# Optimization experiments

Hardware: AMD Instinct MI355X
Metric: run time of the kernel (lower is better)

Reference implementation:

```python
import jax, jax.numpy as jnp
import numpy as np

N_NODES = 50000
N_EDGES = 800000
HIDDEN = 64


def _init_linear(key, fan_in, fan_out):
    kw, kb = jax.random.split(key)
    lim = 1.0 / np.sqrt(fan_in)
    W = jax.random.uniform(kw, (fan_in, fan_out), jnp.float32, -lim, lim)
    b = jax.random.uniform(kb, (fan_out,), jnp.float32, -lim, lim)
    return W, b


def setup_inputs() -> dict:
    key = jax.random.key(0)
    ks = jax.random.split(key, 10)
    feat = jax.random.normal(ks[0], (N_NODES, HIDDEN), jnp.float32)
    x = jax.random.normal(ks[1], (N_NODES, 3), jnp.float32)
    src = jax.random.randint(ks[2], (N_EDGES,), 0, N_NODES, jnp.int32)
    dst = jax.random.randint(ks[3], (N_EDGES,), 0, N_NODES, jnp.int32)
    # message MLP: (2H+1) -> H -> H, relu after both layers (last_activation=mid)
    W1, b1 = _init_linear(ks[4], 2 * HIDDEN + 1, HIDDEN)
    W2, b2 = _init_linear(ks[5], HIDDEN, HIDDEN)
    # soft edge gate: H -> 1
    we, be = _init_linear(ks[6], HIDDEN, 1)
    # update MLP: H -> H -> H, relu mid, no last activation
    U1, c1 = _init_linear(ks[7], HIDDEN, HIDDEN)
    U2, c2 = _init_linear(ks[8], HIDDEN, HIDDEN)
    return dict(feat=feat, x=x, src=src, dst=dst,
                W1=W1, b1=b1, W2=W2, b2=b2, we=we, be=be,
                U1=U1, c1=c1, U2=U2, c2=c2)


def reference(feat, x, src, dst, W1, b1, W2, b2, we, be, U1, c1, U2, c2):
    # per-edge squared distance between endpoint coordinates: [E, 1]
    sqd = jnp.sum((x[src] - x[dst]) ** 2, axis=-1, keepdims=True)
    # message input: [E, 2H+1]
    msg_in = jnp.concatenate([feat[src], feat[dst], sqd], axis=-1)
    # 2-layer message MLP with relu mid and last activation
    m = jax.nn.relu(jax.nn.relu(msg_in @ W1 + b1) @ W2 + b2)
    # sigmoid soft-edge gate: [E, 1]
    gate = jax.nn.sigmoid(m @ we + be)
    # scatter-sum gated messages to destination nodes: [N, H]
    m_sum = jax.ops.segment_sum(m * gate, dst, num_segments=N_NODES)
    # node update MLP on (m_sum + feat), residual add
    h = m_sum + feat
    h_new = jax.nn.relu(h @ U1 + c1) @ U2 + c2
    return h_new + feat
```

## Files before the change

### kernel.cpp

```cpp
#include <hip/hip_runtime.h>
#include <hip/hip_bf16.h>
#include <stdint.h>

#define N_NODES 50000
#define N_EDGES 800000
#define HDIM 64
#define SCAN_N (N_NODES + 1)

#define MSUM_OFF   0
#define DEG_OFF    12800000
#define ZERO_BYTES (DEG_OFF + 204800)
#define PART_OFF   (DEG_OFF + 204800)
#define OFFS_OFF   (PART_OFF + 1024)
#define POS_OFF    (OFFS_OFF + 204800)
#define EP_OFF     (POS_OFF + 204800)
#define FB_OFF     (EP_OFF + 12800000)
#define W1T_OFF    (FB_OFF + (size_t)N_NODES * HDIM * 2)
#define W2T_OFF    (W1T_OFF + 16384)
#define U1T_OFF    (W2T_OFF + 8192)
#define U2T_OFF    (U1T_OFF + 8192)
#define CST_OFF    (U2T_OFF + 8192)
#define WS_NEED    (CST_OFF + 4096)

#define CVT_BLOCKS   1563
#define PREPW_BLOCKS 82
#define HIST_BLOCKS  1024

typedef __attribute__((ext_vector_type(8))) short short8;
typedef __attribute__((ext_vector_type(4))) float floatx4;

__device__ __forceinline__ float bf2f(unsigned short u) {
    union { unsigned int i; float f; } v; v.i = ((unsigned int)u) << 16; return v.f;
}
__device__ __forceinline__ unsigned short f2bf(float f) {
    __hip_bfloat16 h = __float2bfloat16(f);
    return *reinterpret_cast<unsigned short*>(&h);
}

__device__ __forceinline__ int detect_is_bf16(const unsigned short* p) {
    int cnt = 0;
    #pragma unroll
    for (int i = 0; i < 64; ++i) {
        unsigned short b = p[i];
        int e = (b >> 7) & 0xFF;
        cnt += ((e >= 97 && e <= 157) || (b & 0x7FFF) == 0) ? 1 : 0;
    }
    return cnt >= 56;
}

__device__ __forceinline__ float getf(const void* p, unsigned int i, int isb) {
    return isb ? bf2f(((const unsigned short*)p)[i]) : ((const float*)p)[i];
}

__device__ __forceinline__ short8 get8bf(const void* p, unsigned int i, int isb) {
    if (isb) {
        return *reinterpret_cast<const short8*>((const short*)p + i);
    } else {
        const float4 f0 = *reinterpret_cast<const float4*>((const float*)p + i);
        const float4 f1 = *reinterpret_cast<const float4*>((const float*)p + i + 4);
        short8 a;
        a[0] = (short)f2bf(f0.x); a[1] = (short)f2bf(f0.y);
        a[2] = (short)f2bf(f0.z); a[3] = (short)f2bf(f0.w);
        a[4] = (short)f2bf(f1.x); a[5] = (short)f2bf(f1.y);
        a[6] = (short)f2bf(f1.z); a[7] = (short)f2bf(f1.w);
        return a;
    }
}

#define COMPILER_FENCE() asm volatile("" ::: "memory")
#define WAIT_LDS() __builtin_amdgcn_s_waitcnt(0xC07F)

__global__ __launch_bounds__(256) void prep_kernel(
    const void* __restrict__ feat, unsigned short* __restrict__ fb,
    const void* __restrict__ W1, const void* __restrict__ W2,
    const void* __restrict__ U1, const void* __restrict__ U2,
    const void* __restrict__ b1, const void* __restrict__ b2,
    const void* __restrict__ we, const void* __restrict__ be,
    unsigned short* __restrict__ w1t, unsigned short* __restrict__ w2t,
    unsigned short* __restrict__ u1t, unsigned short* __restrict__ u2t,
    float* __restrict__ cst,
    const int* __restrict__ dst, int* __restrict__ deg)
{
    const int b = blockIdx.x;
    if (b < CVT_BLOCKS) {
        const int isb = detect_is_bf16((const unsigned short*)feat);
        int i = (b * 256 + threadIdx.x) * 8;
        if (i >= N_NODES * HDIM) return;
        if (isb) {
            *reinterpret_cast<uint4*>(fb + i) =
                *reinterpret_cast<const uint4*>((const unsigned short*)feat + i);
        } else {
            float4 f0 = *reinterpret_cast<const float4*>((const float*)feat + i);
            float4 f1 = *reinterpret_cast<const float4*>((const float*)feat + i + 4);
            ushort4 a = {f2bf(f0.x), f2bf(f0.y), f2bf(f0.z), f2bf(f0.w)};
            ushort4 c = {f2bf(f1.x), f2bf(f1.y), f2bf(f1.z), f2bf(f1.w)};
            *reinterpret_cast<ushort4*>(fb + i)     = a;
            *reinterpret_cast<ushort4*>(fb + i + 4) = c;
        }
    } else if (b < CVT_BLOCKS + PREPW_BLOCKS) {
        const int isb = detect_is_bf16((const unsigned short*)feat);
        int idx = (b - CVT_BLOCKS) * 256 + threadIdx.x;
        if (idx < 8192) {
            int n = idx >> 7, k = idx & 127;
            w1t[idx] = f2bf(getf(W1, k * 64 + n, isb));
        } else if (idx < 12288) {
            int i = idx - 8192, n = i >> 6, k = i & 63;
            w2t[i] = f2bf(getf(W2, k * 64 + n, isb));
        } else if (idx < 16384) {
            int i = idx - 12288, n = i >> 6, k = i & 63;
            u1t[i] = f2bf(getf(U1, k * 64 + n, isb));
        } else if (idx < 20480) {
            int i = idx - 16384, n = i >> 6, k = i & 63;
            u2t[i] = f2bf(getf(U2, k * 64 + n, isb));
        } else if (idx < 20737) {
            int i = idx - 20480;
            float v;
            if (i < 64)       v = getf(b1, i, isb);
            else if (i < 128) v = getf(W1, 128 * 64 + (i - 64), isb);
            else if (i < 192) v = getf(b2, i - 128, isb);
            else if (i < 256) v = getf(we, i - 192, isb);
            else              v = getf(be, 0, isb);
            cst[i] = v;
        }
    } else {
        int e0 = (b - CVT_BLOCKS - PREPW_BLOCKS) * 256 + threadIdx.x;
        for (int e = e0; e < N_EDGES; e += HIST_BLOCKS * 256)
            atomicAdd(&deg[dst[e]], 1);
    }
}

__global__ void scan1_kernel(const int* __restrict__ deg, int* __restrict__ part) {
    __shared__ int s[1024];
    int g = blockIdx.x * 1024 + threadIdx.x;
    s[threadIdx.x] = (g < SCAN_N) ? deg[g] : 0;
    __syncthreads();
    for (int off = 512; off > 0; off >>= 1) {
        if (threadIdx.x < off) s[threadIdx.x] += s[threadIdx.x + off];
        __syncthreads();
    }
    if (threadIdx.x == 0) part[blockIdx.x] = s[0];
}

__global__ void scan3_kernel(const int* __restrict__ deg, const int* __restrict__ part,
                             int* __restrict__ offs, int* __restrict__ pos) {
    __shared__ int s[1024];
    __shared__ int sbase;
    if (threadIdx.x < 64) {
        int v = (threadIdx.x < blockIdx.x) ? part[threadIdx.x] : 0;
        #pragma unroll
        for (int off = 32; off >= 1; off >>= 1) v += __shfl_xor(v, off);
        if (threadIdx.x == 0) sbase = v;
    }
    int g = blockIdx.x * 1024 + threadIdx.x;
    int v = (g < SCAN_N) ? deg[g] : 0;
    s[threadIdx.x] = v;
    __syncthreads();
    for (int off = 1; off < 1024; off <<= 1) {
        int t = (threadIdx.x >= off) ? s[threadIdx.x - off] : 0;
        __syncthreads();
        s[threadIdx.x] += t;
        __syncthreads();
    }
    int excl = s[threadIdx.x] - v + sbase;
    if (g < SCAN_N) { offs[g] = excl; pos[g] = excl; }
}

__global__ __launch_bounds__(256) void permute_kernel(
    const void* __restrict__ feat, const void* __restrict__ xpos,
    const int* __restrict__ src, const int* __restrict__ dst,
    int* __restrict__ pos, uint4* __restrict__ epack)
{
    const int isb = detect_is_bf16((const unsigned short*)feat);
    int e = blockIdx.x * 256 + threadIdx.x;
    if (e < N_EDGES) {
        int s = src[e], d = dst[e];
        int slot = atomicAdd(&pos[d], 1);
        float dx = getf(xpos, s * 3 + 0, isb) - getf(xpos, d * 3 + 0, isb);
        float dy = getf(xpos, s * 3 + 1, isb) - getf(xpos, d * 3 + 1, isb);
        float dz = getf(xpos, s * 3 + 2, isb) - getf(xpos, d * 3 + 2, isb);
        float sqd = dx * dx + dy * dy + dz * dz;
        uint4 p;
        p.x = (unsigned int)s;
        p.y = (unsigned int)d;
        p.z = __float_as_uint(sqd);
        p.w = 0u;
        epack[slot] = p;
    }
}

template <bool CSR>
__global__ __launch_bounds__(512, 4) void edge_kernel(
    const unsigned short* __restrict__ fbf,
    const unsigned short* __restrict__ w1t, const unsigned short* __restrict__ w2t,
    const float* __restrict__ cst,
    const void* __restrict__ feat, const void* __restrict__ xpos,
    const int* __restrict__ src, const int* __restrict__ dst,
    const uint4* __restrict__ epack,
    const void* __restrict__ W1, const void* __restrict__ b1,
    const void* __restrict__ W2, const void* __restrict__ b2,
    const void* __restrict__ we, const void* __restrict__ be,
    float* __restrict__ msum, unsigned int msum_cap)
{
    __shared__ __align__(16) short sW1[16][64][8];
    __shared__ __align__(16) short sW2[8][64][8];
    __shared__ __align__(16) short sA2[2][8][16][72];

    const int tid  = threadIdx.x;
    const int wave = tid >> 6;
    const int lane = tid & 63;
    const int l15  = lane & 15;
    const int quad = lane >> 4;
    const int rowb = quad * 4;

    float b1r[4], w1lr[4], b2r[4], wer[4];
    float ber;
    short8 bw1[4][4];
    short8 bw2[2][4];

    if constexpr (CSR) {
        for (int i = tid; i < 16 * 64; i += 512) {
            int f = i >> 6, l = i & 63;
            int n = (f & 3) * 16 + (l & 15);
            int k0 = (f >> 2) * 32 + (l >> 4) * 8;
            *reinterpret_cast<short8*>(&sW1[f][l][0]) =
                *reinterpret_cast<const short8*>(w1t + n * 128 + k0);
        }
        for (int i = tid; i < 8 * 64; i += 512) {
            int f = i >> 6, l = i & 63;
            int n = (f & 3) * 16 + (l & 15);
            int k0 = (f >> 2) * 32 + (l >> 4) * 8;
            *reinterpret_cast<short8*>(&sW2[f][l][0]) =
                *reinterpret_cast<const short8*>(w2t + n * 64 + k0);
        }
        #pragma unroll
        for (int nt = 0; nt < 4; ++nt) {
            int n = nt * 16 + l15;
            b1r[nt]  = cst[n];
            w1lr[nt] = cst[64 + n];
            b2r[nt]  = cst[128 + n];
            wer[nt]  = cst[192 + n];
        }
        ber = cst[256];
        __syncthreads();

        const int nbiter = N_EDGES / 256;
        const int per = (nbiter + (int)gridDim.x - 1) / (int)gridDim.x;
        const int t0 = blockIdx.x * per;
        const int t1 = (t0 + per < nbiter) ? t0 + per : nbiter;
        for (int it = t0; it < t1; ++it) {
            const int ebase = it * 256 + wave * 16;

            int sidx = 0, didx = 0;
            float sqd = 0.f;
            if (lane < 32) {
                int e = ebase + l15 + ((lane >> 4) << 7);
                uint4 p = epack[e];
                sidx = (int)p.x;
                didx = (int)p.y;
                sqd  = __uint_as_float(p.z);
            }
            const int snA = __shfl(sidx, l15);
            const int dnA = __shfl(didx, l15);
            const int snB = __shfl(sidx, l15 + 16);
            const int dnB = __shfl(didx, l15 + 16);

            short8 caA[4], caB[4];
            #pragma unroll
            for (int c = 0; c < 4; ++c) {
                const int nA = (c < 2) ? snA : dnA;
                const int nB = (c < 2) ? snB : dnB;
                caA[c] = *reinterpret_cast<const short8*>(
                    (const short*)fbf + (unsigned int)nA * 64u + (c & 1) * 32 + quad * 8);
                caB[c] = *reinterpret_cast<const short8*>(
                    (const short*)fbf + (unsigned int)nB * 64u + (c & 1) * 32 + quad * 8);
            }

            floatx4 accA[4], accB[4];
            #pragma unroll
            for (int nt = 0; nt < 4; ++nt) {
                accA[nt] = (floatx4){0.f, 0.f, 0.f, 0.f};
                accB[nt] = (floatx4){0.f, 0.f, 0.f, 0.f};
            }
            #pragma unroll
            for (int c = 0; c < 4; ++c) {
                #pragma unroll
                for (int nt = 0; nt < 4; ++nt) {
                    short8 wb = *reinterpret_cast<const short8*>(&sW1[c * 4 + nt][lane][0]);
                    accA[nt] = __builtin_amdgcn_mfma_f32_16x16x32_bf16(caA[c], wb, accA[nt], 0, 0, 0);
                    accB[nt] = __builtin_amdgcn_mfma_f32_16x16x32_bf16(caB[c], wb, accB[nt], 0, 0, 0);
                }
            }

            float sqA[4], sqB[4];
            #pragma unroll
            for (int r = 0; r < 4; ++r) {
                sqA[r] = __shfl(sqd, rowb + r);
                sqB[r] = __shfl(sqd, 16 + rowb + r);
            }
            #pragma unroll
            for (int nt = 0; nt < 4; ++nt)
                #pragma unroll
                for (int r = 0; r < 4; ++r) {
                    float vA = fmaxf(fmaf(sqA[r], w1lr[nt], accA[nt][r]) + b1r[nt], 0.f);
                    float vB = fmaxf(fmaf(sqB[r], w1lr[nt], accB[nt][r]) + b1r[nt], 0.f);
                    sA2[0][wave][rowb + r][nt * 16 + l15] = (short)f2bf(vA);
                    sA2[1][wave][rowb + r][nt * 16 + l15] = (short)f2bf(vB);
                }
            COMPILER_FENCE();
            WAIT_LDS();

            floatx4 acc2A[4], acc2B[4];
            #pragma unroll
            for (int nt = 0; nt < 4; ++nt) {
                acc2A[nt] = (floatx4){0.f, 0.f, 0.f, 0.f};
                acc2B[nt] = (floatx4){0.f, 0.f, 0.f, 0.f};
            }
            #pragma unroll
            for (int c = 0; c < 2; ++c) {
                short8 aA = *reinterpret_cast<const short8*>(&sA2[0][wave][l15][c * 32 + quad * 8]);
                short8 aB = *reinterpret_cast<const short8*>(&sA2[1][wave][l15][c * 32 + quad * 8]);
                #pragma unroll
                for (int nt = 0; nt < 4; ++nt) {
                    short8 wb = *reinterpret_cast<const short8*>(&sW2[c * 4 + nt][lane][0]);
                    acc2A[nt] = __builtin_amdgcn_mfma_f32_16x16x32_bf16(aA, wb, acc2A[nt], 0, 0, 0);
                    acc2B[nt] = __builtin_amdgcn_mfma_f32_16x16x32_bf16(aB, wb, acc2B[nt], 0, 0, 0);
                }
            }
            COMPILER_FENCE();

            float mvA[4][4], mvB[4][4];
            float pA[4] = {0.f, 0.f, 0.f, 0.f};
            float pB[4] = {0.f, 0.f, 0.f, 0.f};
            #pragma unroll
            for (int nt = 0; nt < 4; ++nt)
                #pragma unroll
                for (int r = 0; r < 4; ++r) {
                    float vA = fmaxf(acc2A[nt][r] + b2r[nt], 0.f);
                    float vB = fmaxf(acc2B[nt][r] + b2r[nt], 0.f);
                    mvA[nt][r] = vA;
                    mvB[nt][r] = vB;
                    pA[r] = fmaf(vA, wer[nt], pA[r]);
                    pB[r] = fmaf(vB, wer[nt], pB[r]);
                }
            #pragma unroll
            for (int off = 1; off < 16; off <<= 1)
                #pragma unroll
                for (int r = 0; r < 4; ++r) {
                    pA[r] += __shfl_xor(pA[r], off);
                    pB[r] += __shfl_xor(pB[r], off);
                }
            float gA[4], gB[4];
            #pragma unroll
            for (int r = 0; r < 4; ++r) {
                gA[r] = 1.f / (1.f + __expf(-(pA[r] + ber)));
                gB[r] = 1.f / (1.f + __expf(-(pB[r] + ber)));
            }

            int grp = (lane >> 4) & 1;
            int nd = __shfl(didx, grp * 16 + ((l15 + 1) & 15));
            int flag = (lane < 32) && ((l15 == 15) || (nd != didx));
            unsigned long long bal = __ballot(flag);
            unsigned int mA = (unsigned int)(bal & 0xFFFFull);
            unsigned int mB = (unsigned int)((bal >> 16) & 0xFFFFull);

            int lo = 0;
            while (mA) {
                int hi = __ffs(mA) - 1;
                float s0 = 0.f, s1 = 0.f, s2 = 0.f, s3 = 0.f;
                #pragma unroll
                for (int r = 0; r < 4; ++r) {
                    int gr = rowb + r;
                    float g = (gr >= lo && gr <= hi) ? gA[r] : 0.f;
                    s0 = fmaf(g, mvA[0][r], s0);
                    s1 = fmaf(g, mvA[1][r], s1);
                    s2 = fmaf(g, mvA[2][r], s2);
                    s3 = fmaf(g, mvA[3][r], s3);
                }
                s0 += __shfl_xor(s0, 16); s0 += __shfl_xor(s0, 32);
                s1 += __shfl_xor(s1, 16); s1 += __shfl_xor(s1, 32);
                s2 += __shfl_xor(s2, 16); s2 += __shfl_xor(s2, 32);
                s3 += __shfl_xor(s3, 16); s3 += __shfl_xor(s3, 32);
                int d = __shfl(didx, hi);
                float v = (quad == 0) ? s0 : (quad == 1) ? s1 : (quad == 2) ? s2 : s3;
                unsafeAtomicAdd(&msum[(unsigned int)d * 64u + (unsigned int)quad * 16u + l15], v);
                lo = hi + 1;
                mA &= mA - 1;
            }
            lo = 0;
            while (mB) {
                int hi = __ffs(mB) - 1;
                float s0 = 0.f, s1 = 0.f, s2 = 0.f, s3 = 0.f;
                #pragma unroll
                for (int r = 0; r < 4; ++r) {
                    int gr = rowb + r;
                    float g = (gr >= lo && gr <= hi) ? gB[r] : 0.f;
                    s0 = fmaf(g, mvB[0][r], s0);
                    s1 = fmaf(g, mvB[1][r], s1);
                    s2 = fmaf(g, mvB[2][r], s2);
                    s3 = fmaf(g, mvB[3][r], s3);
                }
                s0 += __shfl_xor(s0, 16); s0 += __shfl_xor(s0, 32);
                s1 += __shfl_xor(s1, 16); s1 += __shfl_xor(s1, 32);
                s2 += __shfl_xor(s2, 16); s2 += __shfl_xor(s2, 32);
                s3 += __shfl_xor(s3, 16); s3 += __shfl_xor(s3, 32);
                int d = __shfl(didx, 16 + hi);
                float v = (quad == 0) ? s0 : (quad == 1) ? s1 : (quad == 2) ? s2 : s3;
                unsafeAtomicAdd(&msum[(unsigned int)d * 64u + (unsigned int)quad * 16u + l15], v);
                lo = hi + 1;
                mB &= mB - 1;
            }
        }
    } else {
        const int isb = detect_is_bf16((const unsigned short*)feat);
        #pragma unroll
        for (int c = 0; c < 4; ++c)
            #pragma unroll
            for (int nt = 0; nt < 4; ++nt) {
                short8 b;
                #pragma unroll
                for (int j = 0; j < 8; ++j)
                    b[j] = (short)f2bf(getf(W1, (c * 32 + quad * 8 + j) * 64 + nt * 16 + l15, isb));
                bw1[c][nt] = b;
            }
        #pragma unroll
        for (int c = 0; c < 2; ++c)
            #pragma unroll
            for (int nt = 0; nt < 4; ++nt) {
                short8 b;
                #pragma unroll
                for (int j = 0; j < 8; ++j)
                    b[j] = (short)f2bf(getf(W2, (c * 32 + quad * 8 + j) * 64 + nt * 16 + l15, isb));
                bw2[c][nt] = b;
            }
        #pragma unroll
        for (int nt = 0; nt < 4; ++nt) {
            int n = nt * 16 + l15;
            b1r[nt]  = getf(b1, n, isb);
            w1lr[nt] = getf(W1, 128 * 64 + n, isb);
            b2r[nt]  = getf(b2, n, isb);
            wer[nt]  = getf(we, n, isb);
        }
        ber = getf(be, 0, isb);

        const int ntiles = N_EDGES / 128;
        for (int t = blockIdx.x; t < ntiles; t += gridDim.x) {
            const int ebase = t * 128 + wave * 16;
            int sidx = 0, didx = 0;
            float sqd = 0.f;
            if (lane < 16) {
                int e = ebase + lane;
                sidx = src[e];
                didx = dst[e];
                float dx = getf(xpos, sidx * 3 + 0, isb) - getf(xpos, didx * 3 + 0, isb);
                float dy = getf(xpos, sidx * 3 + 1, isb) - getf(xpos, didx * 3 + 1, isb);
                float dz = getf(xpos, sidx * 3 + 2, isb) - getf(xpos, didx * 3 + 2, isb);
                sqd = dx * dx + dy * dy + dz * dz;
            }
            const int sn     = __shfl(sidx, l15);
            const int dn_row = __shfl(didx, l15);

            floatx4 acc[4];
            #pragma unroll
            for (int nt = 0; nt < 4; ++nt) acc[nt] = (floatx4){0.f, 0.f, 0.f, 0.f};
            #pragma unroll
            for (int c = 0; c < 4; ++c) {
                const int node = (c < 2) ? sn : dn_row;
                const unsigned int aoff = (unsigned int)node * 64u + (c & 1) * 32 + quad * 8;
                short8 a = get8bf(feat, aoff, isb);
                #pragma unroll
                for (int nt = 0; nt < 4; ++nt)
                    acc[nt] = __builtin_amdgcn_mfma_f32_16x16x32_bf16(a, bw1[c][nt], acc[nt], 0, 0, 0);
            }

            float sq[4];
            #pragma unroll
            for (int r = 0; r < 4; ++r) sq[r] = __shfl(sqd, rowb + r);
            #pragma unroll
            for (int nt = 0; nt < 4; ++nt)
                #pragma unroll
                for (int r = 0; r < 4; ++r) {
                    float v = fmaxf(acc[nt][r] + b1r[nt] + sq[r] * w1lr[nt], 0.f);
                    sA2[0][wave][rowb + r][nt * 16 + l15] = (short)f2bf(v);
                }
            COMPILER_FENCE();
            WAIT_LDS();

            floatx4 acc2[4];
            #pragma unroll
            for (int nt = 0; nt < 4; ++nt) acc2[nt] = (floatx4){0.f, 0.f, 0.f, 0.f};
            #pragma unroll
            for (int c = 0; c < 2; ++c) {
                short8 a = *reinterpret_cast<const short8*>(&sA2[0][wave][l15][c * 32 + quad * 8]);
                #pragma unroll
                for (int nt = 0; nt < 4; ++nt)
                    acc2[nt] = __builtin_amdgcn_mfma_f32_16x16x32_bf16(a, bw2[c][nt], acc2[nt], 0, 0, 0);
            }
            COMPILER_FENCE();
            WAIT_LDS();

            float mval[4][4];
            float part[4] = {0.f, 0.f, 0.f, 0.f};
            #pragma unroll
            for (int nt = 0; nt < 4; ++nt)
                #pragma unroll
                for (int r = 0; r < 4; ++r) {
                    float v = fmaxf(acc2[nt][r] + b2r[nt], 0.f);
                    mval[nt][r] = v;
                    part[r] += v * wer[nt];
                }
            #pragma unroll
            for (int off = 1; off < 16; off <<= 1)
                #pragma unroll
                for (int r = 0; r < 4; ++r) part[r] += __shfl_xor(part[r], off);
            float gate[4];
            #pragma unroll
            for (int r = 0; r < 4; ++r)
                gate[r] = 1.f / (1.f + __expf(-(part[r] + ber)));

            #pragma unroll
            for (int r = 0; r < 4; ++r) {
                int dn = __shfl(didx, rowb + r);
                unsigned int base = (unsigned int)dn * 64u;
                if (base + 64u <= msum_cap) {
                    #pragma unroll
                    for (int nt = 0; nt < 4; ++nt)
                        unsafeAtomicAdd(&msum[base + nt * 16 + l15], mval[nt][r] * gate[r]);
                }
            }
        }
    }
}

__global__ __launch_bounds__(256, 2) void node_kernel(
    const float* __restrict__ msum,
    const unsigned short* __restrict__ u1t, const unsigned short* __restrict__ u2t,
    const void* __restrict__ feat,
    const void* __restrict__ U1, const void* __restrict__ c1v,
    const void* __restrict__ U2, const void* __restrict__ c2v,
    void* __restrict__ out)
{
    __shared__ __align__(16) short sT[4][16][72];
    __shared__ __align__(16) float sF[4][16][68];

    const int isb  = detect_is_bf16((const unsigned short*)feat);
    const int tid  = threadIdx.x;
    const int wave = tid >> 6;
    const int lane = tid & 63;
    const int l15  = lane & 15;
    const int quad = lane >> 4;

    short8 u1f[2][4], u2f[2][4];
    if (u1t) {
        #pragma unroll
        for (int nt = 0; nt < 4; ++nt) {
            const int n = nt * 16 + l15;
            #pragma unroll
            for (int c = 0; c < 2; ++c) {
                u1f[c][nt] = *reinterpret_cast<const short8*>(u1t + n * 64 + c * 32 + quad * 8);
                u2f[c][nt] = *reinterpret_cast<const short8*>(u2t + n * 64 + c * 32 + quad * 8);
            }
        }
    } else {
        #pragma unroll
        for (int c = 0; c < 2; ++c)
            #pragma unroll
            for (int nt = 0; nt < 4; ++nt) {
                short8 a, b;
                #pragma unroll
                for (int j = 0; j < 8; ++j) {
                    int k = c * 32 + quad * 8 + j, n = nt * 16 + l15;
                    a[j] = (short)f2bf(getf(U1, k * 64 + n, isb));
                    b[j] = (short)f2bf(getf(U2, k * 64 + n, isb));
                }
                u1f[c][nt] = a; u2f[c][nt] = b;
            }
    }
    float c1r[4], c2r[4];
    #pragma unroll
    for (int nt = 0; nt < 4; ++nt) {
        c1r[nt] = getf(c1v, nt * 16 + l15, isb);
        c2r[nt] = getf(c2v, nt * 16 + l15, isb);
    }
    const int rowb = quad * 4;

    const int ntile = (N_NODES + 15) / 16;
    const int t = blockIdx.x * 4 + wave;
    if (t < ntile) {
        const int node = t * 16 + l15;

        short8 ah[2];
        #pragma unroll
        for (int c = 0; c < 2; ++c) {
            unsigned int off = (unsigned int)node * 64u + c * 32 + quad * 8;
            float4 m0 = *reinterpret_cast<const float4*>(msum + off);
            float4 m1 = *reinterpret_cast<const float4*>(msum + off + 4);
            float mv[8] = {m0.x, m0.y, m0.z, m0.w, m1.x, m1.y, m1.z, m1.w};
            float hv[8];
            if (isb) {
                short8 fv = *reinterpret_cast<const short8*>((const short*)feat + off);
                #pragma unroll
                for (int j = 0; j < 8; ++j) hv[j] = bf2f((unsigned short)fv[j]);
            } else {
                float4 f0 = *reinterpret_cast<const float4*>((const float*)feat + off);
                float4 f1 = *reinterpret_cast<const float4*>((const float*)feat + off + 4);
                hv[0] = f0.x; hv[1] = f0.y; hv[2] = f0.z; hv[3] = f0.w;
                hv[4] = f1.x; hv[5] = f1.y; hv[6] = f1.z; hv[7] = f1.w;
            }
            short8 a;
            #pragma unroll
            for (int j = 0; j < 8; ++j) a[j] = (short)f2bf(mv[j] + hv[j]);
            ah[c] = a;
        }

        floatx4 acc[4];
        #pragma unroll
        for (int nt = 0; nt < 4; ++nt) acc[nt] = (floatx4){0.f, 0.f, 0.f, 0.f};
        #pragma unroll
        for (int c = 0; c < 2; ++c)
            #pragma unroll
            for (int nt = 0; nt < 4; ++nt)
                acc[nt] = __builtin_amdgcn_mfma_f32_16x16x32_bf16(ah[c], u1f[c][nt], acc[nt], 0, 0, 0);

        #pragma unroll
        for (int nt = 0; nt < 4; ++nt)
            #pragma unroll
            for (int r = 0; r < 4; ++r) {
                float v = fmaxf(acc[nt][r] + c1r[nt], 0.f);
                sT[wave][rowb + r][nt * 16 + l15] = (short)f2bf(v);
            }
        COMPILER_FENCE();
        WAIT_LDS();

        floatx4 acc2[4];
        #pragma unroll
        for (int nt = 0; nt < 4; ++nt) acc2[nt] = (floatx4){0.f, 0.f, 0.f, 0.f};
        #pragma unroll
        for (int c = 0; c < 2; ++c) {
            short8 a = *reinterpret_cast<const short8*>(&sT[wave][l15][c * 32 + quad * 8]);
            #pragma unroll
            for (int nt = 0; nt < 4; ++nt)
                acc2[nt] = __builtin_amdgcn_mfma_f32_16x16x32_bf16(a, u2f[c][nt], acc2[nt], 0, 0, 0);
        }
        COMPILER_FENCE();

        #pragma unroll
        for (int nt = 0; nt < 4; ++nt)
            #pragma unroll
            for (int r = 0; r < 4; ++r)
                sF[wave][rowb + r][nt * 16 + l15] = acc2[nt][r] + c2r[nt];
        COMPILER_FENCE();
        WAIT_LDS();

        const unsigned int ob = (unsigned int)node * 64u + quad * 16;
        if (isb) {
            const unsigned short* fp = (const unsigned short*)feat + ob;
            unsigned short* op = (unsigned short*)out + ob;
            #pragma unroll
            for (int k = 0; k < 2; ++k) {
                ushort4 o0, o1;
                float4 v0 = *reinterpret_cast<const float4*>(&sF[wave][l15][quad * 16 + k * 8]);
                float4 v1 = *reinterpret_cast<const float4*>(&sF[wave][l15][quad * 16 + k * 8 + 4]);
                const ushort4 f0 = *reinterpret_cast<const ushort4*>(fp + k * 8);
                const ushort4 f1 = *reinterpret_cast<const ushort4*>(fp + k * 8 + 4);
                o0.x = f2bf(v0.x + bf2f(f0.x)); o0.y = f2bf(v0.y + bf2f(f0.y));
                o0.z = f2bf(v0.z + bf2f(f0.z)); o0.w = f2bf(v0.w + bf2f(f0.w));
                o1.x = f2bf(v1.x + bf2f(f1.x)); o1.y = f2bf(v1.y + bf2f(f1.y));
                o1.z = f2bf(v1.z + bf2f(f1.z)); o1.w = f2bf(v1.w + bf2f(f1.w));
                *reinterpret_cast<ushort4*>(op + k * 8)     = o0;
                *reinterpret_cast<ushort4*>(op + k * 8 + 4) = o1;
            }
        } else {
            const float* fp = (const float*)feat + ob;
            float* op = (float*)out + ob;
            #pragma unroll
            for (int k = 0; k < 4; ++k) {
                float4 v = *reinterpret_cast<const float4*>(&sF[wave][l15][quad * 16 + k * 4]);
                float4 f = *reinterpret_cast<const float4*>(fp + k * 4);
                float4 o = {v.x + f.x, v.y + f.y, v.z + f.z, v.w + f.w};
                *reinterpret_cast<float4*>(op + k * 4) = o;
            }
        }
        COMPILER_FENCE();
    }
}

extern "C" void kernel_launch(void* const* d_in, const int* in_sizes, int n_in,
                              void* d_out, int out_size, void* d_ws, size_t ws_size,
                              hipStream_t stream) {
    const void* feat = d_in[0];
    const void* x    = d_in[1];
    const int* src   = (const int*)d_in[2];
    const int* dst   = (const int*)d_in[3];
    const void* W1   = d_in[4];
    const void* b1   = d_in[5];
    const void* W2   = d_in[6];
    const void* b2   = d_in[7];
    const void* we   = d_in[8];
    const void* be   = d_in[9];
    const void* U1   = d_in[10];
    const void* c1   = d_in[11];
    const void* U2   = d_in[12];
    const void* c2   = d_in[13];
    char* ws = (char*)d_ws;

    if (ws_size >= WS_NEED) {
        float* msum = (float*)(ws + MSUM_OFF);
        int* deg  = (int*)(ws + DEG_OFF);
        int* part = (int*)(ws + PART_OFF);
        int* offs = (int*)(ws + OFFS_OFF);
        int* pos  = (int*)(ws + POS_OFF);
        uint4* epack = (uint4*)(ws + EP_OFF);
        unsigned short* fb  = (unsigned short*)(ws + FB_OFF);
        unsigned short* w1t = (unsigned short*)(ws + W1T_OFF);
        unsigned short* w2t = (unsigned short*)(ws + W2T_OFF);
        unsigned short* u1t = (unsigned short*)(ws + U1T_OFF);
        unsigned short* u2t = (unsigned short*)(ws + U2T_OFF);
        float* cst = (float*)(ws + CST_OFF);

        hipMemsetAsync(ws, 0, ZERO_BYTES, stream);
        prep_kernel<<<CVT_BLOCKS + PREPW_BLOCKS + HIST_BLOCKS, 256, 0, stream>>>(
            feat, fb, W1, W2, U1, U2, b1, b2, we, be,
            w1t, w2t, u1t, u2t, cst, dst, deg);
        scan1_kernel<<<49, 1024, 0, stream>>>(deg, part);
        scan3_kernel<<<49, 1024, 0, stream>>>(deg, part, offs, pos);
        permute_kernel<<<(N_EDGES + 255) / 256, 256, 0, stream>>>(feat, x, src, dst, pos, epack);
        edge_kernel<true><<<625, 512, 0, stream>>>(fb, w1t, w2t, cst, feat, x, src, dst, epack,
                                                   W1, b1, W2, b2, we, be,
                                                   msum, (unsigned int)(N_NODES * HDIM));
        node_kernel<<<((N_NODES + 15) / 16 + 3) / 4, 256, 0, stream>>>(
            msum, u1t, u2t, feat, U1, c1, U2, c2, d_out);
    } else {
        float* msum = (float*)ws;
        size_t need = (size_t)N_NODES * HDIM * sizeof(float);
        size_t clr  = need < ws_size ? need : ws_size;
        unsigned int cap = (unsigned int)(ws_size / sizeof(float));
        if (cap > (unsigned int)(N_NODES * HDIM)) cap = (unsigned int)(N_NODES * HDIM);

        hipMemsetAsync(msum, 0, clr, stream);
        edge_kernel<false><<<1250, 512, 0, stream>>>(nullptr, nullptr, nullptr, nullptr,
                                                     feat, x, src, dst,
                                                     nullptr, W1, b1, W2, b2, we, be,
                                                     msum, cap);
        node_kernel<<<((N_NODES + 15) / 16 + 3) / 4, 256, 0, stream>>>(
            msum, nullptr, nullptr, feat, U1, c1, U2, c2, d_out);
    }
}
```

Before: 257.4 us.

## Drop CSR sort pipeline and scatter edge messages directly with atomics

Removes the degree histogram, two scan kernels and the permute pass that sorted edges by destination. The edge kernel now reads src/dst in original order, computes squared distance inline, and does per-edge float atomic adds instead of segmented reduction by destination. This saves three kernel launches and the packed edge buffer traffic, but multiplies the number of atomics, since consecutive edges no longer share a destination. The grid also changes to 512 blocks with a strided loop.

```diff
diff --git a/kernel.cpp b/kernel.cpp
--- a/kernel.cpp
+++ b/kernel.cpp
@@ -5,16 +5,10 @@
 #define N_NODES 50000
 #define N_EDGES 800000
 #define HDIM 64
-#define SCAN_N (N_NODES + 1)
 
 #define MSUM_OFF   0
-#define DEG_OFF    12800000
-#define ZERO_BYTES (DEG_OFF + 204800)
-#define PART_OFF   (DEG_OFF + 204800)
-#define OFFS_OFF   (PART_OFF + 1024)
-#define POS_OFF    (OFFS_OFF + 204800)
-#define EP_OFF     (POS_OFF + 204800)
-#define FB_OFF     (EP_OFF + 12800000)
+#define ZERO_BYTES 12800000
+#define FB_OFF     12800000
 #define W1T_OFF    (FB_OFF + (size_t)N_NODES * HDIM * 2)
 #define W2T_OFF    (W1T_OFF + 16384)
 #define U1T_OFF    (W2T_OFF + 8192)
@@ -24,7 +18,6 @@
 
 #define CVT_BLOCKS   1563
 #define PREPW_BLOCKS 82
-#define HIST_BLOCKS  1024
 
 typedef __attribute__((ext_vector_type(8))) short short8;
 typedef __attribute__((ext_vector_type(4))) float floatx4;
@@ -78,8 +71,7 @@
     const void* __restrict__ we, const void* __restrict__ be,
     unsigned short* __restrict__ w1t, unsigned short* __restrict__ w2t,
     unsigned short* __restrict__ u1t, unsigned short* __restrict__ u2t,
-    float* __restrict__ cst,
-    const int* __restrict__ dst, int* __restrict__ deg)
+    float* __restrict__ cst)
 {
     const int b = blockIdx.x;
     if (b < CVT_BLOCKS) {
@@ -97,7 +89,7 @@
             *reinterpret_cast<ushort4*>(fb + i)     = a;
             *reinterpret_cast<ushort4*>(fb + i + 4) = c;
         }
-    } else if (b < CVT_BLOCKS + PREPW_BLOCKS) {
+    } else {
         const int isb = detect_is_bf16((const unsigned short*)feat);
         int idx = (b - CVT_BLOCKS) * 256 + threadIdx.x;
         if (idx < 8192) {
@@ -112,79 +104,17 @@
         } else if (idx < 20480) {
             int i = idx - 16384, n = i >> 6, k = i & 63;
             u2t[i] = f2bf(getf(U2, k * 64 + n, isb));
-        } else if (idx < 20737) {
+        } else if (idx < 20738) {
             int i = idx - 20480;
             float v;
             if (i < 64)       v = getf(b1, i, isb);
             else if (i < 128) v = getf(W1, 128 * 64 + (i - 64), isb);
             else if (i < 192) v = getf(b2, i - 128, isb);
             else if (i < 256) v = getf(we, i - 192, isb);
-            else              v = getf(be, 0, isb);
+            else if (i == 256) v = getf(be, 0, isb);
+            else              v = (float)isb;
             cst[i] = v;
         }
-    } else {
-        int e0 = (b - CVT_BLOCKS - PREPW_BLOCKS) * 256 + threadIdx.x;
-        for (int e = e0; e < N_EDGES; e += HIST_BLOCKS * 256)
-            atomicAdd(&deg[dst[e]], 1);
-    }
-}
-
-__global__ void scan1_kernel(const int* __restrict__ deg, int* __restrict__ part) {
-    __shared__ int s[1024];
-    int g = blockIdx.x * 1024 + threadIdx.x;
-    s[threadIdx.x] = (g < SCAN_N) ? deg[g] : 0;
-    __syncthreads();
-    for (int off = 512; off > 0; off >>= 1) {
-        if (threadIdx.x < off) s[threadIdx.x] += s[threadIdx.x + off];
-        __syncthreads();
-    }
-    if (threadIdx.x == 0) part[blockIdx.x] = s[0];
-}
-
-__global__ void scan3_kernel(const int* __restrict__ deg, const int* __restrict__ part,
-                             int* __restrict__ offs, int* __restrict__ pos) {
-    __shared__ int s[1024];
-    __shared__ int sbase;
-    if (threadIdx.x < 64) {
-        int v = (threadIdx.x < blockIdx.x) ? part[threadIdx.x] : 0;
-        #pragma unroll
-        for (int off = 32; off >= 1; off >>= 1) v += __shfl_xor(v, off);
-        if (threadIdx.x == 0) sbase = v;
-    }
-    int g = blockIdx.x * 1024 + threadIdx.x;
-    int v = (g < SCAN_N) ? deg[g] : 0;
-    s[threadIdx.x] = v;
-    __syncthreads();
-    for (int off = 1; off < 1024; off <<= 1) {
-        int t = (threadIdx.x >= off) ? s[threadIdx.x - off] : 0;
-        __syncthreads();
-        s[threadIdx.x] += t;
-        __syncthreads();
-    }
-    int excl = s[threadIdx.x] - v + sbase;
-    if (g < SCAN_N) { offs[g] = excl; pos[g] = excl; }
-}
-
-__global__ __launch_bounds__(256) void permute_kernel(
-    const void* __restrict__ feat, const void* __restrict__ xpos,
-    const int* __restrict__ src, const int* __restrict__ dst,
-    int* __restrict__ pos, uint4* __restrict__ epack)
-{
-    const int isb = detect_is_bf16((const unsigned short*)feat);
-    int e = blockIdx.x * 256 + threadIdx.x;
-    if (e < N_EDGES) {
-        int s = src[e], d = dst[e];
-        int slot = atomicAdd(&pos[d], 1);
-        float dx = getf(xpos, s * 3 + 0, isb) - getf(xpos, d * 3 + 0, isb);
-        float dy = getf(xpos, s * 3 + 1, isb) - getf(xpos, d * 3 + 1, isb);
-        float dz = getf(xpos, s * 3 + 2, isb) - getf(xpos, d * 3 + 2, isb);
-        float sqd = dx * dx + dy * dy + dz * dz;
-        uint4 p;
-        p.x = (unsigned int)s;
-        p.y = (unsigned int)d;
-        p.z = __float_as_uint(sqd);
-        p.w = 0u;
-        epack[slot] = p;
     }
 }
 
@@ -195,7 +125,6 @@
     const float* __restrict__ cst,
     const void* __restrict__ feat, const void* __restrict__ xpos,
     const int* __restrict__ src, const int* __restrict__ dst,
-    const uint4* __restrict__ epack,
     const void* __restrict__ W1, const void* __restrict__ b1,
     const void* __restrict__ W2, const void* __restrict__ b2,
     const void* __restrict__ we, const void* __restrict__ be,
@@ -241,23 +170,23 @@
             wer[nt]  = cst[192 + n];
         }
         ber = cst[256];
+        const int isb = (int)cst[257];
         __syncthreads();
 
         const int nbiter = N_EDGES / 256;
-        const int per = (nbiter + (int)gridDim.x - 1) / (int)gridDim.x;
-        const int t0 = blockIdx.x * per;
-        const int t1 = (t0 + per < nbiter) ? t0 + per : nbiter;
-        for (int it = t0; it < t1; ++it) {
+        for (int it = blockIdx.x; it < nbiter; it += gridDim.x) {
             const int ebase = it * 256 + wave * 16;
 
             int sidx = 0, didx = 0;
             float sqd = 0.f;
             if (lane < 32) {
                 int e = ebase + l15 + ((lane >> 4) << 7);
-                uint4 p = epack[e];
-                sidx = (int)p.x;
-                didx = (int)p.y;
-                sqd  = __uint_as_float(p.z);
+                sidx = src[e];
+                didx = dst[e];
+                float dx = getf(xpos, sidx * 3 + 0, isb) - getf(xpos, didx * 3 + 0, isb);
+                float dy = getf(xpos, sidx * 3 + 1, isb) - getf(xpos, didx * 3 + 1, isb);
+                float dz = getf(xpos, sidx * 3 + 2, isb) - getf(xpos, didx * 3 + 2, isb);
+                sqd = dx * dx + dy * dy + dz * dz;
             }
             const int snA = __shfl(sidx, l15);
             const int dnA = __shfl(didx, l15);
@@ -356,58 +285,21 @@
                 gB[r] = 1.f / (1.f + __expf(-(pB[r] + ber)));
             }
 
-            int grp = (lane >> 4) & 1;
-            int nd = __shfl(didx, grp * 16 + ((l15 + 1) & 15));
-            int flag = (lane < 32) && ((l15 == 15) || (nd != didx));
-            unsigned long long bal = __ballot(flag);
-            unsigned int mA = (unsigned int)(bal & 0xFFFFull);
-            unsigned int mB = (unsigned int)((bal >> 16) & 0xFFFFull);
-
-            int lo = 0;
-            while (mA) {
-                int hi = __ffs(mA) - 1;
-                float s0 = 0.f, s1 = 0.f, s2 = 0.f, s3 = 0.f;
-                #pragma unroll
-                for (int r = 0; r < 4; ++r) {
-                    int gr = rowb + r;
-                    float g = (gr >= lo && gr <= hi) ? gA[r] : 0.f;
-                    s0 = fmaf(g, mvA[0][r], s0);
-                    s1 = fmaf(g, mvA[1][r], s1);
-                    s2 = fmaf(g, mvA[2][r], s2);
-                    s3 = fmaf(g, mvA[3][r], s3);
-                }
-                s0 += __shfl_xor(s0, 16); s0 += __shfl_xor(s0, 32);
-                s1 += __shfl_xor(s1, 16); s1 += __shfl_xor(s1, 32);
-                s2 += __shfl_xor(s2, 16); s2 += __shfl_xor(s2, 32);
-                s3 += __shfl_xor(s3, 16); s3 += __shfl_xor(s3, 32);
-                int d = __shfl(didx, hi);
-                float v = (quad == 0) ? s0 : (quad == 1) ? s1 : (quad == 2) ? s2 : s3;
-                unsafeAtomicAdd(&msum[(unsigned int)d * 64u + (unsigned int)quad * 16u + l15], v);
-                lo = hi + 1;
-                mA &= mA - 1;
-            }
-            lo = 0;
-            while (mB) {
-                int hi = __ffs(mB) - 1;
-                float s0 = 0.f, s1 = 0.f, s2 = 0.f, s3 = 0.f;
-                #pragma unroll
-                for (int r = 0; r < 4; ++r) {
-                    int gr = rowb + r;
-                    float g = (gr >= lo && gr <= hi) ? gB[r] : 0.f;
-                    s0 = fmaf(g, mvB[0][r], s0);
-                    s1 = fmaf(g, mvB[1][r], s1);
-                    s2 = fmaf(g, mvB[2][r], s2);
-                    s3 = fmaf(g, mvB[3][r], s3);
-                }
-                s0 += __shfl_xor(s0, 16); s0 += __shfl_xor(s0, 32);
-                s1 += __shfl_xor(s1, 16); s1 += __shfl_xor(s1, 32);
-                s2 += __shfl_xor(s2, 16); s2 += __shfl_xor(s2, 32);
-                s3 += __shfl_xor(s3, 16); s3 += __shfl_xor(s3, 32);
-                int d = __shfl(didx, 16 + hi);
-                float v = (quad == 0) ? s0 : (quad == 1) ? s1 : (quad == 2) ? s2 : s3;
-                unsafeAtomicAdd(&msum[(unsigned int)d * 64u + (unsigned int)quad * 16u + l15], v);
-                lo = hi + 1;
-                mB &= mB - 1;
+            #pragma unroll
+            for (int r = 0; r < 4; ++r) {
+                int dA = __shfl(didx, rowb + r);
+                unsigned int baseA = (unsigned int)dA * 64u;
+                #pragma unroll
+                for (int nt = 0; nt < 4; ++nt)
+                    unsafeAtomicAdd(&msum[baseA + nt * 16 + l15], mvA[nt][r] * gA[r]);
+            }
+            #pragma unroll
+            for (int r = 0; r < 4; ++r) {
+                int dB = __shfl(didx, 16 + rowb + r);
+                unsigned int baseB = (unsigned int)dB * 64u;
+                #pragma unroll
+                for (int nt = 0; nt < 4; ++nt)
+                    unsafeAtomicAdd(&msum[baseB + nt * 16 + l15], mvB[nt][r] * gB[r]);
             }
         }
     } else {
@@ -705,11 +597,6 @@
 
     if (ws_size >= WS_NEED) {
         float* msum = (float*)(ws + MSUM_OFF);
-        int* deg  = (int*)(ws + DEG_OFF);
-        int* part = (int*)(ws + PART_OFF);
-        int* offs = (int*)(ws + OFFS_OFF);
-        int* pos  = (int*)(ws + POS_OFF);
-        uint4* epack = (uint4*)(ws + EP_OFF);
         unsigned short* fb  = (unsigned short*)(ws + FB_OFF);
         unsigned short* w1t = (unsigned short*)(ws + W1T_OFF);
         unsigned short* w2t = (unsigned short*)(ws + W2T_OFF);
@@ -718,13 +605,10 @@
         float* cst = (float*)(ws + CST_OFF);
 
         hipMemsetAsync(ws, 0, ZERO_BYTES, stream);
-        prep_kernel<<<CVT_BLOCKS + PREPW_BLOCKS + HIST_BLOCKS, 256, 0, stream>>>(
+        prep_kernel<<<CVT_BLOCKS + PREPW_BLOCKS, 256, 0, stream>>>(
             feat, fb, W1, W2, U1, U2, b1, b2, we, be,
-            w1t, w2t, u1t, u2t, cst, dst, deg);
-        scan1_kernel<<<49, 1024, 0, stream>>>(deg, part);
-        scan3_kernel<<<49, 1024, 0, stream>>>(deg, part, offs, pos);
-        permute_kernel<<<(N_EDGES + 255) / 256, 256, 0, stream>>>(feat, x, src, dst, pos, epack);
-        edge_kernel<true><<<625, 512, 0, stream>>>(fb, w1t, w2t, cst, feat, x, src, dst, epack,
+            w1t, w2t, u1t, u2t, cst);
+        edge_kernel<true><<<512, 512, 0, stream>>>(fb, w1t, w2t, cst, feat, x, src, dst,
                                                    W1, b1, W2, b2, we, be,
                                                    msum, (unsigned int)(N_NODES * HDIM));
         node_kernel<<<((N_NODES + 15) / 16 + 3) / 4, 256, 0, stream>>>(
@@ -739,7 +623,7 @@
         hipMemsetAsync(msum, 0, clr, stream);
         edge_kernel<false><<<1250, 512, 0, stream>>>(nullptr, nullptr, nullptr, nullptr,
                                                      feat, x, src, dst,
-                                                     nullptr, W1, b1, W2, b2, we, be,
+                                                     W1, b1, W2, b2, we, be,
                                                      msum, cap);
         node_kernel<<<((N_NODES + 15) / 16 + 3) / 4, 256, 0, stream>>>(
             msum, nullptr, nullptr, feat, U1, c1, U2, c2, d_out);
```

New measurement: 299.3 us. 1.16x slower.
